# Kernel tuning notes

Measured on AMD Instinct MI355X. Metric: run time of the kernel, lower is better.

The kernel has to match this reference:

```python
import jax, jax.numpy as jnp
import numpy as np
import math

B, S, H = 2, 2048, 1024
NH, HD = 16, 64
EPS = 1e-12


def setup_inputs() -> dict:
    key = jax.random.key(0)
    ks = jax.random.split(key, 6)
    scale = 1.0 / math.sqrt(H)
    return {
        "hidden_states": jax.random.normal(ks[0], (B, S, H), jnp.float32),
        "Wq": jax.random.normal(ks[1], (H, H), jnp.float32) * scale,
        "bq": jnp.zeros((H,), jnp.float32),
        "Wk": jax.random.normal(ks[2], (H, H), jnp.float32) * scale,
        "bk": jnp.zeros((H,), jnp.float32),
        "Wv": jax.random.normal(ks[3], (H, H), jnp.float32) * scale,
        "bv": jnp.zeros((H,), jnp.float32),
        "Wo": jax.random.normal(ks[4], (H, H), jnp.float32) * scale,
        "bo": jnp.zeros((H,), jnp.float32),
        "gamma": jnp.ones((H,), jnp.float32),
        "beta": jnp.zeros((H,), jnp.float32),
    }


def _heads(x):
    # [B, S, H] -> [B, NH, S, HD]
    return x.reshape(B, S, NH, HD).transpose(0, 2, 1, 3)


def reference(hidden_states, Wq, bq, Wk, bk, Wv, bv, Wo, bo, gamma, beta):
    q = _heads(hidden_states @ Wq + bq)
    k = _heads(hidden_states @ Wk + bk)
    v = _heads(hidden_states @ Wv + bv)
    # scores: [B, NH, S, S]
    scores = jnp.einsum("bhqd,bhkd->bhqk", q, k) / math.sqrt(HD)
    probs = jax.nn.softmax(scores, axis=-1)
    ctx = jnp.einsum("bhqk,bhkd->bhqd", probs, v)
    ctx = ctx.transpose(0, 2, 1, 3).reshape(B, S, H)
    attn_out = ctx @ Wo + bo
    x = attn_out + hidden_states
    mu = jnp.mean(x, axis=-1, keepdims=True)
    var = jnp.var(x, axis=-1, keepdims=True)
    return (x - mu) / jnp.sqrt(var + EPS) * gamma + beta
```

## Files before the change

kernel.cpp:

```cpp
#include <hip/hip_runtime.h>
#include <hip/hip_bf16.h>

#define B_ 2
#define S_ 2048
#define H_ 1024
#define NH_ 16
#define HD_ 64
#define M_ (B_*S_)

typedef __attribute__((ext_vector_type(8))) short bf16x8;
typedef __attribute__((ext_vector_type(4))) short bf16x4;
typedef __attribute__((ext_vector_type(4))) float f32x4;
typedef __attribute__((ext_vector_type(4))) int   i32x4;

__device__ inline float waveReduceSum(float v) {
#pragma unroll
  for (int off = 32; off >= 1; off >>= 1) v += __shfl_xor(v, off);
  return v;
}

__device__ inline short f2bf(float f) {
  union { float f; unsigned u; } v; v.f = f;
  unsigned r = v.u + 0x7fffu + ((v.u >> 16) & 1u);
  return (short)(r >> 16);
}

__device__ inline unsigned cvt_pk_bf16(float lo, float hi) {
  unsigned w;
  asm("v_cvt_pk_bf16_f32 %0, %1, %2" : "=v"(w) : "v"(lo), "v"(hi));
  return w;
}

__device__ inline void async_load16(const void* g, void* l) {
  __builtin_amdgcn_global_load_lds(
      (const __attribute__((address_space(1))) void*)g,
      (__attribute__((address_space(3))) void*)l, 16, 0, 0);
}

__device__ inline int swz8(int r) { return (r & 3) | (((r >> 3) & 1) << 2); }

__global__ __launch_bounds__(256)
void cvt_bf16(const float* __restrict__ in, short* __restrict__ out) {
  const size_t i = (size_t)blockIdx.x * 256 + threadIdx.x;
  float4 v = ((const float4*)in)[i];
  bf16x4 o;
  o[0] = f2bf(v.x); o[1] = f2bf(v.y); o[2] = f2bf(v.z); o[3] = f2bf(v.w);
  ((bf16x4*)out)[i] = o;
}

__global__ __launch_bounds__(256)
void transpose_w4(const float* __restrict__ W0, const float* __restrict__ W1,
                  const float* __restrict__ W2, const float* __restrict__ W3,
                  short* __restrict__ Tqkv, short* __restrict__ To) {
  const float* W; short* T;
  switch (blockIdx.z) {
    case 0: W = W0; T = Tqkv; break;
    case 1: W = W1; T = Tqkv + (size_t)1024 * 1024; break;
    case 2: W = W2; T = Tqkv + (size_t)2048 * 1024; break;
    default: W = W3; T = To; break;
  }
  __shared__ float tile[32][36];
  const int tid = threadIdx.x;
  const int tx = tid & 7, ty = tid >> 3;
  const int k0 = blockIdx.y << 5, n0 = blockIdx.x << 5;
  float4 v = *(const float4*)&W[(size_t)(k0 + ty) * H_ + n0 + (tx << 2)];
  tile[ty][(tx << 2) + 0] = v.x;
  tile[ty][(tx << 2) + 1] = v.y;
  tile[ty][(tx << 2) + 2] = v.z;
  tile[ty][(tx << 2) + 3] = v.w;
  __syncthreads();
  bf16x4 o;
  o[0] = f2bf(tile[(tx << 2) + 0][ty]);
  o[1] = f2bf(tile[(tx << 2) + 1][ty]);
  o[2] = f2bf(tile[(tx << 2) + 2][ty]);
  o[3] = f2bf(tile[(tx << 2) + 3][ty]);
  *(bf16x4*)&T[(size_t)(n0 + ty) * H_ + k0 + (tx << 2)] = o;
}

__global__ __launch_bounds__(256)
void gemm_qkv(const short* __restrict__ A, const short* __restrict__ Bt,
              const float* __restrict__ bq, const float* __restrict__ bk,
              const float* __restrict__ bv, short* __restrict__ Qo,
              short* __restrict__ Ko, short* __restrict__ Vto) {
  __shared__ short A_lds[2][128][32];
  __shared__ short B_lds[2][128][32];
  const int tid = threadIdx.x;
  const int lane = tid & 63, wv = tid >> 6;
  const int l16 = lane & 15, lg = lane >> 4;
  const int wr = wv >> 1, wc = wv & 1;
  const int swzb = (blockIdx.x & 7) * 96 + (blockIdx.x >> 3);
  const int bx = swzb % 24, by = swzb / 24;
  const int m0 = by << 7, n0 = bx << 7;
  const int K = H_;

  const int srow = lane >> 2, soff = (lane & 3) << 3;

  f32x4 acc[4][4] = {};

#pragma unroll
  for (int i = 0; i < 2; ++i) {
    const int c = 2 * wv + i;
    async_load16(A + (size_t)(m0 + 16 * c + srow) * K + soff, &A_lds[0][16 * c][0]);
    async_load16(Bt + (size_t)(n0 + 16 * c + srow) * K + soff, &B_lds[0][16 * c][0]);
  }

  int cur = 0;
  for (int t = 0; t < K / 32; ++t) {
    __syncthreads();
    if (t + 1 < K / 32) {
      const int k0 = (t + 1) << 5;
#pragma unroll
      for (int i = 0; i < 2; ++i) {
        const int c = 2 * wv + i;
        async_load16(A + (size_t)(m0 + 16 * c + srow) * K + k0 + soff,
                     &A_lds[cur ^ 1][16 * c][0]);
        async_load16(Bt + (size_t)(n0 + 16 * c + srow) * K + k0 + soff,
                     &B_lds[cur ^ 1][16 * c][0]);
      }
    }
    bf16x8 af[4], bfr[4];
#pragma unroll
    for (int i = 0; i < 4; ++i)
      af[i] = *(const bf16x8*)&A_lds[cur][64 * wr + 16 * i + l16][8 * lg];
#pragma unroll
    for (int j = 0; j < 4; ++j)
      bfr[j] = *(const bf16x8*)&B_lds[cur][64 * wc + 16 * j + l16][8 * lg];
#pragma unroll
    for (int i = 0; i < 4; ++i)
#pragma unroll
      for (int j = 0; j < 4; ++j)
        acc[i][j] = __builtin_amdgcn_mfma_f32_16x16x32_bf16(af[i], bfr[j], acc[i][j], 0, 0, 0);
    cur ^= 1;
  }

  const int mt = n0 >> 10;
  const float* bias = (mt == 0) ? bq : (mt == 1 ? bk : bv);
  const float qs = (mt == 0) ? 0.125f * 1.4426950408889634f : 1.0f;

  if (mt < 2) {
    short* Out = (mt == 0) ? Qo : Ko;
#pragma unroll
    for (int i = 0; i < 4; ++i) {
#pragma unroll
      for (int j = 0; j < 4; ++j) {
        const int nl = (n0 & 1023) + 64 * wc + 16 * j + l16;
        const float bvl = bias[nl];
        const int h = nl >> 6, d = nl & 63;
#pragma unroll
        for (int r = 0; r < 4; ++r) {
          const int m = m0 + 64 * wr + 16 * i + 4 * lg + r;
          const int b = m >> 11, s = m & (S_ - 1);
          Out[(((size_t)(b * NH_ + h) * S_ + s) << 6) + d] =
              f2bf((acc[i][j][r] + bvl) * qs);
        }
      }
    }
  } else {
#pragma unroll
    for (int i = 0; i < 4; ++i) {
      const int mb = m0 + 64 * wr + 16 * i + 4 * lg;
      const int b = mb >> 11, s = mb & (S_ - 1);
#pragma unroll
      for (int j = 0; j < 4; ++j) {
        const int nl = (n0 & 1023) + 64 * wc + 16 * j + l16;
        const float bvl = bias[nl];
        const int h = nl >> 6, d = nl & 63;
        bf16x4 pk;
#pragma unroll
        for (int r = 0; r < 4; ++r) pk[r] = f2bf(acc[i][j][r] + bvl);
        *(bf16x4*)&Vto[(((size_t)(b * NH_ + h) * HD_ + d) << 11) + s] = pk;
      }
    }
  }
}

__global__ __launch_bounds__(256)
void gemm_o(const short* __restrict__ A, const short* __restrict__ Bt,
            const float* __restrict__ bias, float* __restrict__ C) {
  __shared__ short A_lds[2][128][32];
  __shared__ short B_lds[2][128][32];
  const int tid = threadIdx.x;
  const int lane = tid & 63, wv = tid >> 6;
  const int l16 = lane & 15, lg = lane >> 4;
  const int wr = wv >> 1, wc = wv & 1;
  const int swzb = (blockIdx.x & 7) * 32 + (blockIdx.x >> 3);
  const int bx = swzb & 7, by = swzb >> 3;
  const int m0 = by << 7, n0 = bx << 7;
  const int K = H_;

  const int srow = lane >> 2, soff = (lane & 3) << 3;

  f32x4 acc[4][4] = {};

#pragma unroll
  for (int i = 0; i < 2; ++i) {
    const int c = 2 * wv + i;
    async_load16(A + (size_t)(m0 + 16 * c + srow) * K + soff, &A_lds[0][16 * c][0]);
    async_load16(Bt + (size_t)(n0 + 16 * c + srow) * K + soff, &B_lds[0][16 * c][0]);
  }

  int cur = 0;
  for (int t = 0; t < K / 32; ++t) {
    __syncthreads();
    if (t + 1 < K / 32) {
      const int k0 = (t + 1) << 5;
#pragma unroll
      for (int i = 0; i < 2; ++i) {
        const int c = 2 * wv + i;
        async_load16(A + (size_t)(m0 + 16 * c + srow) * K + k0 + soff,
                     &A_lds[cur ^ 1][16 * c][0]);
        async_load16(Bt + (size_t)(n0 + 16 * c + srow) * K + k0 + soff,
                     &B_lds[cur ^ 1][16 * c][0]);
      }
    }
    bf16x8 af[4], bfr[4];
#pragma unroll
    for (int i = 0; i < 4; ++i)
      af[i] = *(const bf16x8*)&A_lds[cur][64 * wr + 16 * i + l16][8 * lg];
#pragma unroll
    for (int j = 0; j < 4; ++j)
      bfr[j] = *(const bf16x8*)&B_lds[cur][64 * wc + 16 * j + l16][8 * lg];
#pragma unroll
    for (int i = 0; i < 4; ++i)
#pragma unroll
      for (int j = 0; j < 4; ++j)
        acc[i][j] = __builtin_amdgcn_mfma_f32_16x16x32_bf16(af[i], bfr[j], acc[i][j], 0, 0, 0);
    cur ^= 1;
  }

#pragma unroll
  for (int i = 0; i < 4; ++i)
#pragma unroll
    for (int j = 0; j < 4; ++j) {
      const int n = n0 + 64 * wc + 16 * j + l16;
      const float bvl = bias[n];
#pragma unroll
      for (int r = 0; r < 4; ++r) {
        const int m = m0 + 64 * wr + 16 * i + 4 * lg + r;
        C[(size_t)m * H_ + n] = acc[i][j][r] + bvl;
      }
    }
}

#define KVB 64

__global__ __launch_bounds__(256)
void attn_mfma(const short* __restrict__ Qg, const short* __restrict__ Kg,
               const short* __restrict__ Vtg, short* __restrict__ ctxb) {
  __shared__ short K_lds[2][KVB][64];
  __shared__ short V_t[2][KVB][64];

  const int tid  = threadIdx.x;
  const int lane = tid & 63;
  const int wv   = tid >> 6;
  const int l16  = lane & 15, lg = lane >> 4;

  const int swz = (blockIdx.x & 7) * 128 + (blockIdx.x >> 3);
  const int bh = swz >> 5, qb = swz & 31;

  const short* Qh = Qg + ((size_t)bh * S_ << 6);
  const short* Kh = Kg + ((size_t)bh * S_ << 6);
  const short* Vh = Vtg + ((size_t)bh << 6) * S_;

  const int q0 = qb * 64 + wv * 16;

  bf16x8 qf[2];
  qf[0] = *(const bf16x8*)&Qh[((size_t)(q0 + l16) << 6) + 8 * lg];
  qf[1] = *(const bf16x8*)&Qh[((size_t)(q0 + l16) << 6) + 8 * lg + 32];

  const int l16part = ((l16 >> 2) << 3) + (l16 & 3);

  const int kr = tid >> 2;
  const int cb = (tid & 3) << 1;
  const int sz = swz8(kr);
  const int c1 = ((cb    ) ^ sz) << 3;
  const int c2 = ((cb + 1) ^ sz) << 3;

  f32x4 o[4] = {};
  float m_run = -1e30f, l_run = 0.f;

  {
    *(bf16x8*)&K_lds[0][kr][c1] = *(const bf16x8*)&Kh[((size_t)kr << 6) + (cb << 3)];
    *(bf16x8*)&K_lds[0][kr][c2] = *(const bf16x8*)&Kh[((size_t)kr << 6) + ((cb + 1) << 3)];
    *(bf16x8*)&V_t[0][kr][c1]   = *(const bf16x8*)&Vh[(size_t)kr * S_ + (cb << 3)];
    *(bf16x8*)&V_t[0][kr][c2]   = *(const bf16x8*)&Vh[(size_t)kr * S_ + ((cb + 1) << 3)];
  }

  int cur = 0;
  for (int t = 0; t < S_ / KVB; ++t) {
    bf16x8 nk0, nk1, nv0, nv1;
    const bool pre = (t + 1 < S_ / KVB);
    if (pre) {
      const size_t kb = (size_t)((t + 1) * KVB + kr) << 6;
      nk0 = *(const bf16x8*)&Kh[kb + (cb << 3)];
      nk1 = *(const bf16x8*)&Kh[kb + ((cb + 1) << 3)];
      const size_t vb = (size_t)kr * S_ + (t + 1) * KVB;
      nv0 = *(const bf16x8*)&Vh[vb + (cb << 3)];
      nv1 = *(const bf16x8*)&Vh[vb + ((cb + 1) << 3)];
    }
    __syncthreads();

    f32x4 s[4] = {};
#pragma unroll
    for (int ks = 0; ks < 2; ++ks)
#pragma unroll
      for (int tt = 0; tt < 4; ++tt) {
        const int krow = ((tt >> 1) << 5) + ((tt & 1) << 2) + l16part;
        const int kch = (lg + 4 * ks) ^ swz8(krow);
        bf16x8 kf = *(const bf16x8*)&K_lds[cur][krow][kch << 3];
        s[tt] = __builtin_amdgcn_mfma_f32_16x16x32_bf16(kf, qf[ks], s[tt], 0, 0, 0);
      }

    float pmax = fmaxf(fmaxf(fmaxf(s[0][0], s[0][1]), fmaxf(s[0][2], s[0][3])),
                       fmaxf(fmaxf(s[1][0], s[1][1]), fmaxf(s[1][2], s[1][3])));
    pmax = fmaxf(pmax,
                 fmaxf(fmaxf(fmaxf(s[2][0], s[2][1]), fmaxf(s[2][2], s[2][3])),
                       fmaxf(fmaxf(s[3][0], s[3][1]), fmaxf(s[3][2], s[3][3]))));
    pmax = fmaxf(pmax, __shfl_xor(pmax, 16));
    pmax = fmaxf(pmax, __shfl_xor(pmax, 32));

    float p[4][4];
    float rs = 0.f;
    if (__any(pmax - m_run > 8.0f)) {
      const float mn = fmaxf(m_run, pmax);
      const float scl = __builtin_amdgcn_exp2f(m_run - mn);
      m_run = mn;
#pragma unroll
      for (int tt = 0; tt < 4; ++tt)
#pragma unroll
        for (int r = 0; r < 4; ++r) {
          p[tt][r] = __builtin_amdgcn_exp2f(s[tt][r] - mn);
          rs += p[tt][r];
        }
      rs += __shfl_xor(rs, 16);
      rs += __shfl_xor(rs, 32);
      l_run = l_run * scl + rs;
      float sclr[4];
#pragma unroll
      for (int r = 0; r < 4; ++r) sclr[r] = __shfl(scl, 4 * lg + r);
#pragma unroll
      for (int tt = 0; tt < 4; ++tt)
#pragma unroll
        for (int r = 0; r < 4; ++r) o[tt][r] *= sclr[r];
    } else {
#pragma unroll
      for (int tt = 0; tt < 4; ++tt)
#pragma unroll
        for (int r = 0; r < 4; ++r) {
          p[tt][r] = __builtin_amdgcn_exp2f(s[tt][r] - m_run);
          rs += p[tt][r];
        }
      rs += __shfl_xor(rs, 16);
      rs += __shfl_xor(rs, 32);
      l_run += rs;
    }

    unsigned w[4][2];
#pragma unroll
    for (int tt = 0; tt < 4; ++tt) {
      w[tt][0] = cvt_pk_bf16(p[tt][0], p[tt][1]);
      w[tt][1] = cvt_pk_bf16(p[tt][2], p[tt][3]);
    }

#pragma unroll
    for (int ks = 0; ks < 2; ++ks) {
      i32x4 aw;
      aw[0] = (int)w[2 * ks][0];
      aw[1] = (int)w[2 * ks][1];
      aw[2] = (int)w[2 * ks + 1][0];
      aw[3] = (int)w[2 * ks + 1][1];
      const bf16x8 pf = __builtin_bit_cast(bf16x8, aw);
#pragma unroll
      for (int tt = 0; tt < 4; ++tt) {
        const int vrow = 16 * tt + l16;
        const int vch = (lg + 4 * ks) ^ swz8(vrow);
        bf16x8 vf = *(const bf16x8*)&V_t[cur][vrow][vch << 3];
        o[tt] = __builtin_amdgcn_mfma_f32_16x16x32_bf16(pf, vf, o[tt], 0, 0, 0);
      }
    }

    if (pre) {
      *(bf16x8*)&K_lds[cur ^ 1][kr][c1] = nk0;
      *(bf16x8*)&K_lds[cur ^ 1][kr][c2] = nk1;
      *(bf16x8*)&V_t[cur ^ 1][kr][c1]   = nv0;
      *(bf16x8*)&V_t[cur ^ 1][kr][c2]   = nv1;
    }
    cur ^= 1;
  }

  float invr[4];
#pragma unroll
  for (int r = 0; r < 4; ++r) invr[r] = 1.f / __shfl(l_run, 4 * lg + r);
  const int b = bh >> 4, h = bh & 15;
#pragma unroll
  for (int r = 0; r < 4; ++r) {
    const int q = q0 + 4 * lg + r;
#pragma unroll
    for (int tt = 0; tt < 4; ++tt)
      ctxb[(((size_t)(b * S_ + q) * NH_ + h) << 6) + 16 * tt + l16] =
          f2bf(o[tt][r] * invr[r]);
  }
}

__global__ __launch_bounds__(256)
void resid_ln(const float* __restrict__ attn_out, const float* __restrict__ hs,
              const float* __restrict__ gamma, const float* __restrict__ beta,
              float* __restrict__ out) {
  __shared__ float reds[4], reds2[4];
  const int row = blockIdx.x;
  const int tid = threadIdx.x;
  const float4* a4 = (const float4*)(attn_out + ((size_t)row << 10));
  const float4* h4 = (const float4*)(hs + ((size_t)row << 10));
  float4 a = a4[tid], h = h4[tid];
  float e0 = a.x + h.x, e1 = a.y + h.y, e2 = a.z + h.z, e3 = a.w + h.w;
  float s  = e0 + e1 + e2 + e3;
  float sq = e0 * e0 + e1 * e1 + e2 * e2 + e3 * e3;
  s = waveReduceSum(s);
  sq = waveReduceSum(sq);
  const int lane = tid & 63, wave = tid >> 6;
  if (lane == 0) { reds[wave] = s; reds2[wave] = sq; }
  __syncthreads();
  const float S1 = reds[0] + reds[1] + reds[2] + reds[3];
  const float S2 = reds2[0] + reds2[1] + reds2[2] + reds2[3];
  const float mu = S1 * (1.f / H_);
  const float var = S2 * (1.f / H_) - mu * mu;
  const float rstd = rsqrtf(var + 1e-12f);
  const float4 g = ((const float4*)gamma)[tid];
  const float4 bb = ((const float4*)beta)[tid];
  float4 o;
  o.x = (e0 - mu) * rstd * g.x + bb.x;
  o.y = (e1 - mu) * rstd * g.y + bb.y;
  o.z = (e2 - mu) * rstd * g.z + bb.z;
  o.w = (e3 - mu) * rstd * g.w + bb.w;
  ((float4*)(out + ((size_t)row << 10)))[tid] = o;
}

extern "C" void kernel_launch(void* const* d_in, const int* in_sizes, int n_in,
                              void* d_out, int out_size, void* d_ws, size_t ws_size,
                              hipStream_t stream) {
  const float* X     = (const float*)d_in[0];
  const float* Wq    = (const float*)d_in[1];
  const float* bq    = (const float*)d_in[2];
  const float* Wk    = (const float*)d_in[3];
  const float* bk    = (const float*)d_in[4];
  const float* Wv    = (const float*)d_in[5];
  const float* bv    = (const float*)d_in[6];
  const float* Wo    = (const float*)d_in[7];
  const float* bo    = (const float*)d_in[8];
  const float* gamma = (const float*)d_in[9];
  const float* beta  = (const float*)d_in[10];
  float* out = (float*)d_out;

  char* ws = (char*)d_ws;
  short* Xbf  = (short*)ws;
  short* Wqkv = (short*)(ws + ( 8u << 20));
  short* Wto  = (short*)(ws + (14u << 20));
  short* Qbf  = (short*)(ws + (16u << 20));
  short* Kbf  = (short*)(ws + (24u << 20));
  short* Vt   = (short*)(ws + (32u << 20));
  short* ctxb = Xbf;
  float* attn = (float*)(ws + (16u << 20));

  dim3 blk(256);
  hipLaunchKernelGGL(cvt_bf16, dim3((M_ * H_) / 1024), blk, 0, stream, X, Xbf);
  hipLaunchKernelGGL(transpose_w4, dim3(32, 32, 4), blk, 0, stream,
                     Wq, Wk, Wv, Wo, Wqkv, Wto);
  hipLaunchKernelGGL(gemm_qkv, dim3(768), blk, 0, stream,
                     Xbf, Wqkv, bq, bk, bv, Qbf, Kbf, Vt);
  hipLaunchKernelGGL(attn_mfma, dim3(1024), blk, 0, stream, Qbf, Kbf, Vt, ctxb);
  hipLaunchKernelGGL(gemm_o, dim3(256), blk, 0, stream, ctxb, Wto, bo, attn);
  hipLaunchKernelGGL(resid_ln, dim3(M_), blk, 0, stream, attn, X, gamma, beta, out);
}
```

Baseline: 256.4 us.

## Double attention KV tile to 128 keys, add MFMA priority, halve gemm_o M tile

The attention kernel now loads and processes 128 keys per iteration as two 64-key halves. This halves the number of barriers and softmax rescale checks per query block. The QK and PV MFMA sections are wrapped in s_setprio to favour matrix issue over other waves. Separately, the output projection GEMM now uses 64x128 tiles on a 512-block grid so more CUs are busy, at the cost of re-reading B tiles more often. The larger attention tile increases LDS use and registers per thread, which could reduce occupancy.

```diff
diff --git a/kernel.cpp b/kernel.cpp
--- a/kernel.cpp
+++ b/kernel.cpp
@@ -177,25 +177,25 @@
 __global__ __launch_bounds__(256)
 void gemm_o(const short* __restrict__ A, const short* __restrict__ Bt,
             const float* __restrict__ bias, float* __restrict__ C) {
-  __shared__ short A_lds[2][128][32];
+  __shared__ short A_lds[2][64][32];
   __shared__ short B_lds[2][128][32];
   const int tid = threadIdx.x;
   const int lane = tid & 63, wv = tid >> 6;
   const int l16 = lane & 15, lg = lane >> 4;
   const int wr = wv >> 1, wc = wv & 1;
-  const int swzb = (blockIdx.x & 7) * 32 + (blockIdx.x >> 3);
+  const int swzb = (blockIdx.x & 7) * 64 + (blockIdx.x >> 3);
   const int bx = swzb & 7, by = swzb >> 3;
-  const int m0 = by << 7, n0 = bx << 7;
+  const int m0 = by << 6, n0 = bx << 7;
   const int K = H_;
 
   const int srow = lane >> 2, soff = (lane & 3) << 3;
 
-  f32x4 acc[4][4] = {};
-
+  f32x4 acc[2][4] = {};
+
+  async_load16(A + (size_t)(m0 + 16 * wv + srow) * K + soff, &A_lds[0][16 * wv][0]);
 #pragma unroll
   for (int i = 0; i < 2; ++i) {
     const int c = 2 * wv + i;
-    async_load16(A + (size_t)(m0 + 16 * c + srow) * K + soff, &A_lds[0][16 * c][0]);
     async_load16(Bt + (size_t)(n0 + 16 * c + srow) * K + soff, &B_lds[0][16 * c][0]);
   }
 
@@ -204,24 +204,24 @@
     __syncthreads();
     if (t + 1 < K / 32) {
       const int k0 = (t + 1) << 5;
+      async_load16(A + (size_t)(m0 + 16 * wv + srow) * K + k0 + soff,
+                   &A_lds[cur ^ 1][16 * wv][0]);
 #pragma unroll
       for (int i = 0; i < 2; ++i) {
         const int c = 2 * wv + i;
-        async_load16(A + (size_t)(m0 + 16 * c + srow) * K + k0 + soff,
-                     &A_lds[cur ^ 1][16 * c][0]);
         async_load16(Bt + (size_t)(n0 + 16 * c + srow) * K + k0 + soff,
                      &B_lds[cur ^ 1][16 * c][0]);
       }
     }
-    bf16x8 af[4], bfr[4];
-#pragma unroll
-    for (int i = 0; i < 4; ++i)
-      af[i] = *(const bf16x8*)&A_lds[cur][64 * wr + 16 * i + l16][8 * lg];
+    bf16x8 af[2], bfr[4];
+#pragma unroll
+    for (int i = 0; i < 2; ++i)
+      af[i] = *(const bf16x8*)&A_lds[cur][32 * wr + 16 * i + l16][8 * lg];
 #pragma unroll
     for (int j = 0; j < 4; ++j)
       bfr[j] = *(const bf16x8*)&B_lds[cur][64 * wc + 16 * j + l16][8 * lg];
 #pragma unroll
-    for (int i = 0; i < 4; ++i)
+    for (int i = 0; i < 2; ++i)
 #pragma unroll
       for (int j = 0; j < 4; ++j)
         acc[i][j] = __builtin_amdgcn_mfma_f32_16x16x32_bf16(af[i], bfr[j], acc[i][j], 0, 0, 0);
@@ -229,26 +229,24 @@
   }
 
 #pragma unroll
-  for (int i = 0; i < 4; ++i)
+  for (int i = 0; i < 2; ++i)
 #pragma unroll
     for (int j = 0; j < 4; ++j) {
       const int n = n0 + 64 * wc + 16 * j + l16;
       const float bvl = bias[n];
 #pragma unroll
       for (int r = 0; r < 4; ++r) {
-        const int m = m0 + 64 * wr + 16 * i + 4 * lg + r;
+        const int m = m0 + 32 * wr + 16 * i + 4 * lg + r;
         C[(size_t)m * H_ + n] = acc[i][j][r] + bvl;
       }
     }
 }
-
-#define KVB 64
 
 __global__ __launch_bounds__(256)
 void attn_mfma(const short* __restrict__ Qg, const short* __restrict__ Kg,
                const short* __restrict__ Vtg, short* __restrict__ ctxb) {
-  __shared__ short K_lds[2][KVB][64];
-  __shared__ short V_t[2][KVB][64];
+  __shared__ short K_lds[2][2][64][64];
+  __shared__ short V_t[2][2][64][64];
 
   const int tid  = threadIdx.x;
   const int lane = tid & 63;
@@ -279,59 +277,74 @@
   f32x4 o[4] = {};
   float m_run = -1e30f, l_run = 0.f;
 
-  {
-    *(bf16x8*)&K_lds[0][kr][c1] = *(const bf16x8*)&Kh[((size_t)kr << 6) + (cb << 3)];
-    *(bf16x8*)&K_lds[0][kr][c2] = *(const bf16x8*)&Kh[((size_t)kr << 6) + ((cb + 1) << 3)];
-    *(bf16x8*)&V_t[0][kr][c1]   = *(const bf16x8*)&Vh[(size_t)kr * S_ + (cb << 3)];
-    *(bf16x8*)&V_t[0][kr][c2]   = *(const bf16x8*)&Vh[(size_t)kr * S_ + ((cb + 1) << 3)];
+#pragma unroll
+  for (int h = 0; h < 2; ++h) {
+    const size_t kg = ((size_t)(64 * h + kr)) << 6;
+    *(bf16x8*)&K_lds[0][h][kr][c1] = *(const bf16x8*)&Kh[kg + (cb << 3)];
+    *(bf16x8*)&K_lds[0][h][kr][c2] = *(const bf16x8*)&Kh[kg + ((cb + 1) << 3)];
+    const size_t vg = (size_t)kr * S_ + 64 * h;
+    *(bf16x8*)&V_t[0][h][kr][c1]   = *(const bf16x8*)&Vh[vg + (cb << 3)];
+    *(bf16x8*)&V_t[0][h][kr][c2]   = *(const bf16x8*)&Vh[vg + ((cb + 1) << 3)];
   }
 
   int cur = 0;
-  for (int t = 0; t < S_ / KVB; ++t) {
-    bf16x8 nk0, nk1, nv0, nv1;
-    const bool pre = (t + 1 < S_ / KVB);
+  for (int t = 0; t < S_ / 128; ++t) {
+    bf16x8 nk[2][2], nv[2][2];
+    const bool pre = (t + 1 < S_ / 128);
     if (pre) {
-      const size_t kb = (size_t)((t + 1) * KVB + kr) << 6;
-      nk0 = *(const bf16x8*)&Kh[kb + (cb << 3)];
-      nk1 = *(const bf16x8*)&Kh[kb + ((cb + 1) << 3)];
-      const size_t vb = (size_t)kr * S_ + (t + 1) * KVB;
-      nv0 = *(const bf16x8*)&Vh[vb + (cb << 3)];
-      nv1 = *(const bf16x8*)&Vh[vb + ((cb + 1) << 3)];
+      const int kvn = (t + 1) * 128;
+#pragma unroll
+      for (int h = 0; h < 2; ++h) {
+        const size_t kb = ((size_t)(kvn + 64 * h + kr)) << 6;
+        nk[h][0] = *(const bf16x8*)&Kh[kb + (cb << 3)];
+        nk[h][1] = *(const bf16x8*)&Kh[kb + ((cb + 1) << 3)];
+        const size_t vb = (size_t)kr * S_ + kvn + 64 * h;
+        nv[h][0] = *(const bf16x8*)&Vh[vb + (cb << 3)];
+        nv[h][1] = *(const bf16x8*)&Vh[vb + ((cb + 1) << 3)];
+      }
     }
     __syncthreads();
 
-    f32x4 s[4] = {};
-#pragma unroll
-    for (int ks = 0; ks < 2; ++ks)
-#pragma unroll
-      for (int tt = 0; tt < 4; ++tt) {
-        const int krow = ((tt >> 1) << 5) + ((tt & 1) << 2) + l16part;
-        const int kch = (lg + 4 * ks) ^ swz8(krow);
-        bf16x8 kf = *(const bf16x8*)&K_lds[cur][krow][kch << 3];
-        s[tt] = __builtin_amdgcn_mfma_f32_16x16x32_bf16(kf, qf[ks], s[tt], 0, 0, 0);
-      }
-
-    float pmax = fmaxf(fmaxf(fmaxf(s[0][0], s[0][1]), fmaxf(s[0][2], s[0][3])),
-                       fmaxf(fmaxf(s[1][0], s[1][1]), fmaxf(s[1][2], s[1][3])));
-    pmax = fmaxf(pmax,
-                 fmaxf(fmaxf(fmaxf(s[2][0], s[2][1]), fmaxf(s[2][2], s[2][3])),
-                       fmaxf(fmaxf(s[3][0], s[3][1]), fmaxf(s[3][2], s[3][3]))));
+    f32x4 s[2][4] = {};
+    __builtin_amdgcn_s_setprio(1);
+#pragma unroll
+    for (int h = 0; h < 2; ++h)
+#pragma unroll
+      for (int ks = 0; ks < 2; ++ks)
+#pragma unroll
+        for (int tt = 0; tt < 4; ++tt) {
+          const int krow = ((tt >> 1) << 5) + ((tt & 1) << 2) + l16part;
+          const int kch = (lg + 4 * ks) ^ swz8(krow);
+          bf16x8 kf = *(const bf16x8*)&K_lds[cur][h][krow][kch << 3];
+          s[h][tt] = __builtin_amdgcn_mfma_f32_16x16x32_bf16(kf, qf[ks], s[h][tt], 0, 0, 0);
+        }
+    __builtin_amdgcn_s_setprio(0);
+
+    float pmax = -1e30f;
+#pragma unroll
+    for (int h = 0; h < 2; ++h)
+#pragma unroll
+      for (int tt = 0; tt < 4; ++tt)
+        pmax = fmaxf(pmax, fmaxf(fmaxf(s[h][tt][0], s[h][tt][1]),
+                                 fmaxf(s[h][tt][2], s[h][tt][3])));
     pmax = fmaxf(pmax, __shfl_xor(pmax, 16));
     pmax = fmaxf(pmax, __shfl_xor(pmax, 32));
 
-    float p[4][4];
+    float p[2][4][4];
     float rs = 0.f;
     if (__any(pmax - m_run > 8.0f)) {
       const float mn = fmaxf(m_run, pmax);
       const float scl = __builtin_amdgcn_exp2f(m_run - mn);
       m_run = mn;
 #pragma unroll
-      for (int tt = 0; tt < 4; ++tt)
-#pragma unroll
-        for (int r = 0; r < 4; ++r) {
-          p[tt][r] = __builtin_amdgcn_exp2f(s[tt][r] - mn);
-          rs += p[tt][r];
-        }
+      for (int h = 0; h < 2; ++h)
+#pragma unroll
+        for (int tt = 0; tt < 4; ++tt)
+#pragma unroll
+          for (int r = 0; r < 4; ++r) {
+            p[h][tt][r] = __builtin_amdgcn_exp2f(s[h][tt][r] - mn);
+            rs += p[h][tt][r];
+          }
       rs += __shfl_xor(rs, 16);
       rs += __shfl_xor(rs, 32);
       l_run = l_run * scl + rs;
@@ -344,46 +357,57 @@
         for (int r = 0; r < 4; ++r) o[tt][r] *= sclr[r];
     } else {
 #pragma unroll
-      for (int tt = 0; tt < 4; ++tt)
-#pragma unroll
-        for (int r = 0; r < 4; ++r) {
-          p[tt][r] = __builtin_amdgcn_exp2f(s[tt][r] - m_run);
-          rs += p[tt][r];
-        }
+      for (int h = 0; h < 2; ++h)
+#pragma unroll
+        for (int tt = 0; tt < 4; ++tt)
+#pragma unroll
+          for (int r = 0; r < 4; ++r) {
+            p[h][tt][r] = __builtin_amdgcn_exp2f(s[h][tt][r] - m_run);
+            rs += p[h][tt][r];
+          }
       rs += __shfl_xor(rs, 16);
       rs += __shfl_xor(rs, 32);
       l_run += rs;
     }
 
-    unsigned w[4][2];
-#pragma unroll
-    for (int tt = 0; tt < 4; ++tt) {
-      w[tt][0] = cvt_pk_bf16(p[tt][0], p[tt][1]);
-      w[tt][1] = cvt_pk_bf16(p[tt][2], p[tt][3]);
-    }
-
-#pragma unroll
-    for (int ks = 0; ks < 2; ++ks) {
-      i32x4 aw;
-      aw[0] = (int)w[2 * ks][0];
-      aw[1] = (int)w[2 * ks][1];
-      aw[2] = (int)w[2 * ks + 1][0];
-      aw[3] = (int)w[2 * ks + 1][1];
-      const bf16x8 pf = __builtin_bit_cast(bf16x8, aw);
+    unsigned w[2][4][2];
+#pragma unroll
+    for (int h = 0; h < 2; ++h)
 #pragma unroll
       for (int tt = 0; tt < 4; ++tt) {
-        const int vrow = 16 * tt + l16;
-        const int vch = (lg + 4 * ks) ^ swz8(vrow);
-        bf16x8 vf = *(const bf16x8*)&V_t[cur][vrow][vch << 3];
-        o[tt] = __builtin_amdgcn_mfma_f32_16x16x32_bf16(pf, vf, o[tt], 0, 0, 0);
-      }
-    }
+        w[h][tt][0] = cvt_pk_bf16(p[h][tt][0], p[h][tt][1]);
+        w[h][tt][1] = cvt_pk_bf16(p[h][tt][2], p[h][tt][3]);
+      }
+
+    __builtin_amdgcn_s_setprio(1);
+#pragma unroll
+    for (int h = 0; h < 2; ++h)
+#pragma unroll
+      for (int ks = 0; ks < 2; ++ks) {
+        i32x4 aw;
+        aw[0] = (int)w[h][2 * ks][0];
+        aw[1] = (int)w[h][2 * ks][1];
+        aw[2] = (int)w[h][2 * ks + 1][0];
+        aw[3] = (int)w[h][2 * ks + 1][1];
+        const bf16x8 pf = __builtin_bit_cast(bf16x8, aw);
+#pragma unroll
+        for (int tt = 0; tt < 4; ++tt) {
+          const int vrow = 16 * tt + l16;
+          const int vch = (lg + 4 * ks) ^ swz8(vrow);
+          bf16x8 vf = *(const bf16x8*)&V_t[cur][h][vrow][vch << 3];
+          o[tt] = __builtin_amdgcn_mfma_f32_16x16x32_bf16(pf, vf, o[tt], 0, 0, 0);
+        }
+      }
+    __builtin_amdgcn_s_setprio(0);
 
     if (pre) {
-      *(bf16x8*)&K_lds[cur ^ 1][kr][c1] = nk0;
-      *(bf16x8*)&K_lds[cur ^ 1][kr][c2] = nk1;
-      *(bf16x8*)&V_t[cur ^ 1][kr][c1]   = nv0;
-      *(bf16x8*)&V_t[cur ^ 1][kr][c2]   = nv1;
+#pragma unroll
+      for (int h = 0; h < 2; ++h) {
+        *(bf16x8*)&K_lds[cur ^ 1][h][kr][c1] = nk[h][0];
+        *(bf16x8*)&K_lds[cur ^ 1][h][kr][c2] = nk[h][1];
+        *(bf16x8*)&V_t[cur ^ 1][h][kr][c1]   = nv[h][0];
+        *(bf16x8*)&V_t[cur ^ 1][h][kr][c2]   = nv[h][1];
+      }
     }
     cur ^= 1;
   }
@@ -468,6 +492,6 @@
   hipLaunchKernelGGL(gemm_qkv, dim3(768), blk, 0, stream,
                      Xbf, Wqkv, bq, bk, bv, Qbf, Kbf, Vt);
   hipLaunchKernelGGL(attn_mfma, dim3(1024), blk, 0, stream, Qbf, Kbf, Vt, ctxb);
-  hipLaunchKernelGGL(gemm_o, dim3(256), blk, 0, stream, ctxb, Wto, bo, attn);
+  hipLaunchKernelGGL(gemm_o, dim3(512), blk, 0, stream, ctxb, Wto, bo, attn);
   hipLaunchKernelGGL(resid_ln, dim3(M_), blk, 0, stream, attn, X, gamma, beta, out);
 }
```

New measurement: 244.4 us. 1.05x faster.
